# Kernel optimization log

Measured on AMD Instinct MI355X. Metric: run time of the kernel, lower is better.

## Reference

```python
import jax, jax.numpy as jnp
import numpy as np

N_HEAD = 12
D_MODEL = 768


def setup_inputs() -> dict:
    key = jax.random.key(0)
    ks = jax.random.split(key, 5)
    B, S, D = 8, 1024, D_MODEL
    return {
        "x": jax.random.normal(ks[0], (B, S, D), dtype=jnp.float32),
        "Wqkv": jax.random.normal(ks[1], (D, 3 * D), dtype=jnp.float32) * 0.02,
        "bqkv": jax.random.normal(ks[2], (3 * D,), dtype=jnp.float32) * 0.02,
        "Wproj": jax.random.normal(ks[3], (D, D), dtype=jnp.float32) * 0.02,
        "bproj": jax.random.normal(ks[4], (D,), dtype=jnp.float32) * 0.02,
    }


def _attention(x, Wqkv, bqkv, Wproj, bproj):
    B, S, D = x.shape
    hd = D // N_HEAD
    qkv = x @ Wqkv + bqkv                      # [B,S,3D]
    q, k, v = jnp.split(qkv, 3, axis=-1)
    # split heads -> [B,H,S,hd]
    def sh(t):
        return t.reshape(B, S, N_HEAD, hd).transpose(0, 2, 1, 3)
    q, k, v = sh(q), sh(k), sh(v)
    scores = jnp.einsum("bhqd,bhkd->bhqk", q, k) / jnp.sqrt(jnp.float32(hd))
    causal = jnp.tril(jnp.ones((S, S), dtype=bool))  # [S,S]
    mask_value = jnp.finfo(scores.dtype).min
    scores = jnp.where(causal[None, None], scores, mask_value)
    attn = jax.nn.softmax(scores, axis=-1)
    # dropout p=0.1 treated as identity (eval mode)
    out = jnp.einsum("bhqk,bhkd->bhqd", attn, v)
    out = out.transpose(0, 2, 1, 3).reshape(B, S, D)  # merge heads
    return out @ Wproj + bproj


def reference(x, Wqkv, bqkv, Wproj, bproj):
    return _attention(x, Wqkv, bqkv, Wproj, bproj)
```

## Files before the change

kernel.cpp:

```cpp
#include <hip/hip_runtime.h>
#include <cstddef>

typedef float f32x4 __attribute__((ext_vector_type(4)));
typedef short s16x4 __attribute__((ext_vector_type(4)));
typedef short s16x8 __attribute__((ext_vector_type(8)));
typedef __bf16 bf16x8 __attribute__((ext_vector_type(8)));

#define NB 8
#define NS 1024
#define ND 768
#define NH 12
#define HD 64

__device__ __forceinline__ unsigned short f2bf(float f) {
  unsigned u = __builtin_bit_cast(unsigned, f);
  u += 0x7fffu + ((u >> 16) & 1u);
  return (unsigned short)(u >> 16);
}

__device__ __forceinline__ f32x4 mfma16(bf16x8 a, bf16x8 b, f32x4 c) {
  return __builtin_amdgcn_mfma_f32_16x16x32_bf16(a, b, c, 0, 0, 0);
}

__device__ __forceinline__ bf16x8 ld8(const unsigned short* p) {
  return *reinterpret_cast<const bf16x8*>(p);
}

__device__ __forceinline__ void gload16(unsigned short* lds_dst, const unsigned short* gsrc) {
  __builtin_amdgcn_global_load_lds(
      (const __attribute__((address_space(1))) unsigned int*)gsrc,
      (__attribute__((address_space(3))) unsigned int*)lds_dst, 16, 0, 0);
}

#define VMW(N) asm volatile("s_waitcnt vmcnt(" #N ")" ::: "memory")


__global__ __launch_bounds__(256) void cvt_f32_bf16(const float* __restrict__ in,
                                                    unsigned short* __restrict__ out) {
  int i = (blockIdx.x * 256 + threadIdx.x) * 4;
  float4 v = *reinterpret_cast<const float4*>(in + i);
  ushort4 o;
  o.x = f2bf(v.x); o.y = f2bf(v.y); o.z = f2bf(v.z); o.w = f2bf(v.w);
  *reinterpret_cast<ushort4*>(out + i) = o;
}

__global__ __launch_bounds__(256) void transpose_cvt(const float* __restrict__ in,
                                                     unsigned short* __restrict__ out,
                                                     int R, int C) {
  __shared__ float tile[32][33];
  int c0 = blockIdx.x * 32, r0 = blockIdx.y * 32;
  int tx = threadIdx.x & 31, ty = threadIdx.x >> 5;
#pragma unroll
  for (int i = 0; i < 32; i += 8)
    tile[ty + i][tx] = in[(size_t)(r0 + ty + i) * C + c0 + tx];
  __syncthreads();
#pragma unroll
  for (int i = 0; i < 32; i += 8)
    out[(size_t)(c0 + ty + i) * R + r0 + tx] = f2bf(tile[tx][ty + i]);
}


#define SLOT 8192

__device__ __forceinline__ void gemm_mainloop4(const unsigned short* __restrict__ A,
                                               const unsigned short* __restrict__ Bt,
                                               int K, int m0, int n0,
                                               unsigned short* smem,
                                               f32x4 (&acc)[4][4]) {
  int tid = threadIdx.x, lane = tid & 63, wid = tid >> 6;
  int wr = wid >> 1, wc = wid & 1;
  int ll = lane & 15, lh = lane >> 4;
  int swsrc = ((lane & 3) ^ ((lane >> 3) & 3)) * 8;

  const unsigned short* asrc = A + (size_t)(m0 + wid * 32 + (lane >> 2)) * K + swsrc;
  const unsigned short* bsrc = Bt + (size_t)(n0 + wid * 32 + (lane >> 2)) * K + swsrc;
  const int sw = (lh ^ ((ll >> 1) & 3)) * 8;
  const int nt = K / 32;

  auto stage = [&](int slot, int t) {
    unsigned short* ad = smem + slot * SLOT + wid * 1024;
    unsigned short* bd = smem + slot * SLOT + 4096 + wid * 1024;
    const unsigned short* as = asrc + t * 32;
    const unsigned short* bs = bsrc + t * 32;
    gload16(ad, as);
    gload16(ad + 512, as + (size_t)16 * K);
    gload16(bd, bs);
    gload16(bd + 512, bs + (size_t)16 * K);
  };

  stage(0, 0);
  stage(1, 1);
  stage(2, 2);
  VMW(8);
  __builtin_amdgcn_s_barrier();
  asm volatile("" ::: "memory");

  for (int t = 0; t < nt; ++t) {
    if (t + 3 < nt) stage((t + 3) & 3, t + 3);

    const unsigned short* Ab = smem + (t & 3) * SLOT;
    const unsigned short* Bb = Ab + 4096;

    __builtin_amdgcn_s_setprio(1);
    bf16x8 af[4], bg[4];
#pragma unroll
    for (int m = 0; m < 4; m++) af[m] = ld8(Ab + (wr * 64 + m * 16 + ll) * 32 + sw);
#pragma unroll
    for (int n = 0; n < 4; n++) bg[n] = ld8(Bb + (wc * 64 + n * 16 + ll) * 32 + sw);
#pragma unroll
    for (int m = 0; m < 4; m++)
#pragma unroll
      for (int n = 0; n < 4; n++) acc[m][n] = mfma16(af[m], bg[n], acc[m][n]);
    __builtin_amdgcn_s_setprio(0);

    if (t + 3 < nt) {
      VMW(8);
      __builtin_amdgcn_s_barrier();
      asm volatile("" ::: "memory");
    } else if (t + 2 < nt) {
      VMW(4);
      __builtin_amdgcn_s_barrier();
      asm volatile("" ::: "memory");
    } else if (t + 1 < nt) {
      VMW(0);
      __builtin_amdgcn_s_barrier();
      asm volatile("" ::: "memory");
    }
  }
}

__device__ __forceinline__ void gemm_mainloop3(const unsigned short* __restrict__ A,
                                               const unsigned short* __restrict__ Bt,
                                               int K, int m0, int n0,
                                               unsigned short* smem,
                                               f32x4 (&acc)[4][4]) {
  int tid = threadIdx.x, lane = tid & 63, wid = tid >> 6;
  int wr = wid >> 1, wc = wid & 1;
  int ll = lane & 15, lh = lane >> 4;
  int swsrc = ((lane & 3) ^ ((lane >> 3) & 3)) * 8;

  const unsigned short* asrc = A + (size_t)(m0 + wid * 32 + (lane >> 2)) * K + swsrc;
  const unsigned short* bsrc = Bt + (size_t)(n0 + wid * 32 + (lane >> 2)) * K + swsrc;
  const int sw = (lh ^ ((ll >> 1) & 3)) * 8;
  const int nt = K / 32;

  auto stage = [&](int slot, int t) {
    unsigned short* ad = smem + slot * SLOT + wid * 1024;
    unsigned short* bd = smem + slot * SLOT + 4096 + wid * 1024;
    const unsigned short* as = asrc + t * 32;
    const unsigned short* bs = bsrc + t * 32;
    gload16(ad, as);
    gload16(ad + 512, as + (size_t)16 * K);
    gload16(bd, bs);
    gload16(bd + 512, bs + (size_t)16 * K);
  };

  stage(0, 0);
  stage(1, 1);
  VMW(4);
  __builtin_amdgcn_s_barrier();
  asm volatile("" ::: "memory");

  int slot = 0;
  for (int t = 0; t < nt; ++t) {
    if (t + 2 < nt) {
      int s2 = slot + 2; if (s2 >= 3) s2 -= 3;
      stage(s2, t + 2);
    }
    const unsigned short* Ab = smem + slot * SLOT;
    const unsigned short* Bb = Ab + 4096;

    __builtin_amdgcn_s_setprio(1);
    bf16x8 af[4], bg[4];
#pragma unroll
    for (int m = 0; m < 4; m++) af[m] = ld8(Ab + (wr * 64 + m * 16 + ll) * 32 + sw);
#pragma unroll
    for (int n = 0; n < 4; n++) bg[n] = ld8(Bb + (wc * 64 + n * 16 + ll) * 32 + sw);
#pragma unroll
    for (int m = 0; m < 4; m++)
#pragma unroll
      for (int n = 0; n < 4; n++) acc[m][n] = mfma16(af[m], bg[n], acc[m][n]);
    __builtin_amdgcn_s_setprio(0);

    if (t + 2 < nt) {
      VMW(4);
      __builtin_amdgcn_s_barrier();
      asm volatile("" ::: "memory");
    } else if (t + 2 == nt) {
      VMW(0);
      __builtin_amdgcn_s_barrier();
      asm volatile("" ::: "memory");
    }
    slot++; if (slot == 3) slot = 0;
  }
}


#define QSCALE 0.18033688f

__global__ __launch_bounds__(256, 2) void qkv_gemm(const unsigned short* __restrict__ xbf,
                                                   const unsigned short* __restrict__ WT,
                                                   const float* __restrict__ bias,
                                                   unsigned short* __restrict__ qw,
                                                   unsigned short* __restrict__ kw,
                                                   unsigned short* __restrict__ vt) {
  __shared__ __align__(16) unsigned short smem[4 * SLOT];
  int bid = blockIdx.x;
  int k8 = bid & 7, j = bid >> 3;
  int m0 = (k8 * 8 + (j & 7)) * 128;
  int n0 = (j >> 3) * 128;
  f32x4 acc[4][4];
#pragma unroll
  for (int m = 0; m < 4; m++)
#pragma unroll
    for (int n = 0; n < 4; n++) acc[m][n] = (f32x4){0.f, 0.f, 0.f, 0.f};

  gemm_mainloop4(xbf, WT, ND, m0, n0, smem, acc);

  int tid = threadIdx.x, lane = tid & 63, wid = tid >> 6;
  int wr = wid >> 1, wc = wid & 1;
  int ll = lane & 15, lh = lane >> 4;
  int which = n0 / ND;

  if (which == 2) {
#pragma unroll
    for (int nf = 0; nf < 4; nf++) {
      int col = n0 + wc * 64 + nf * 16 + ll;
      float bv = bias[col];
      int w2 = col - 2 * ND;
      int h = w2 >> 6, d = w2 & 63;
#pragma unroll
      for (int mf = 0; mf < 4; mf++) {
        int m = m0 + wr * 64 + mf * 16 + lh * 4;
        int b = m >> 10, s = m & 1023;
        s16x4 pk;
        pk[0] = (short)f2bf(acc[mf][nf][0] + bv);
        pk[1] = (short)f2bf(acc[mf][nf][1] + bv);
        pk[2] = (short)f2bf(acc[mf][nf][2] + bv);
        pk[3] = (short)f2bf(acc[mf][nf][3] + bv);
        size_t idx = (((size_t)b * NH + h) * HD + d) * NS + s;
        *(s16x4*)&vt[idx] = pk;
      }
    }
  } else {
#pragma unroll
    for (int nf = 0; nf < 4; nf++) {
      int col = n0 + wc * 64 + nf * 16 + ll;
      float bv = bias[col];
      int w2 = col - which * ND;
      int h = w2 >> 6, d = w2 & 63;
#pragma unroll
      for (int mf = 0; mf < 4; mf++) {
#pragma unroll
        for (int r = 0; r < 4; r++) {
          int m = m0 + wr * 64 + mf * 16 + lh * 4 + r;
          int b = m >> 10, s = m & 1023;
          float v = acc[mf][nf][r] + bv;
          size_t idx = (((size_t)b * NH + h) * NS + s) * HD + d;
          if (which == 0)
            qw[idx] = f2bf(v * QSCALE);
          else
            kw[idx] = f2bf(v);
        }
      }
    }
  }
}


__global__ __launch_bounds__(256, 3) void proj_gemm(const unsigned short* __restrict__ abf,
                                                    const unsigned short* __restrict__ WT,
                                                    const float* __restrict__ bias,
                                                    float* __restrict__ out) {
  __shared__ __align__(16) unsigned short smem[3 * SLOT];
  int bid = blockIdx.x;
  int k8 = bid & 7, j = bid >> 3;
  int m0 = (k8 * 8 + (j & 7)) * 128;
  int n0 = (j >> 3) * 128;
  f32x4 acc[4][4];
#pragma unroll
  for (int m = 0; m < 4; m++)
#pragma unroll
    for (int n = 0; n < 4; n++) acc[m][n] = (f32x4){0.f, 0.f, 0.f, 0.f};

  gemm_mainloop3(abf, WT, ND, m0, n0, smem, acc);

  int tid = threadIdx.x, lane = tid & 63, wid = tid >> 6;
  int wr = wid >> 1, wc = wid & 1;
  int ll = lane & 15, lh = lane >> 4;
#pragma unroll
  for (int nf = 0; nf < 4; nf++) {
    int col = n0 + wc * 64 + nf * 16 + ll;
    float bv = bias[col];
#pragma unroll
    for (int mf = 0; mf < 4; mf++) {
#pragma unroll
      for (int r = 0; r < 4; r++) {
        int m = m0 + wr * 64 + mf * 16 + lh * 4 + r;
        out[(size_t)m * ND + col] = acc[mf][nf][r] + bv;
      }
    }
  }
}


#define LP 88
#define KVSLOT 8192

__global__ __launch_bounds__(512) void attn_kernel(const unsigned short* __restrict__ qw,
                                                   const unsigned short* __restrict__ kw,
                                                   const unsigned short* __restrict__ vt,
                                                   unsigned short* __restrict__ attn_out) {
  int bid = blockIdx.x;
  int xcd = bid & 7, j = bid >> 3;
  int grp = xcd * 12 + (j % 12);
  int qt = 3 - (j / 12);
  int b = grp / NH, h = grp % NH;
  __shared__ __align__(16) unsigned short KV[3 * KVSLOT];
  __shared__ __align__(16) unsigned short Ps[8][16 * LP];

  int tid = threadIdx.x, lane = tid & 63, wid = tid >> 6;
  int ll = lane & 15, lh = lane >> 4, r7x = ll & 7;
  int q0 = qt * 256, q0w = q0 + wid * 32;
  const size_t bhk = ((size_t)b * NH + h) * NS * HD;
  const size_t bhv = ((size_t)b * NH + h) * HD * NS;

  bf16x8 qf[2][2];
#pragma unroll
  for (int g = 0; g < 2; g++) {
    qf[g][0] = ld8(&qw[bhk + (size_t)(q0w + g * 16 + ll) * HD + lh * 8]);
    qf[g][1] = ld8(&qw[bhk + (size_t)(q0w + g * 16 + ll) * HD + 32 + lh * 8]);
  }

  f32x4 o[2][4];
#pragma unroll
  for (int g = 0; g < 2; g++)
#pragma unroll
    for (int n = 0; n < 4; n++) o[g][n] = (f32x4){0.f, 0.f, 0.f, 0.f};
  float m_r[2] = {-1e30f, -1e30f}, l_r[2] = {0.f, 0.f};

  int srow = tid >> 3;
  int scol = ((tid & 7) ^ ((tid >> 3) & 7)) * 8;
  const unsigned short* ksrc = kw + bhk + (size_t)srow * HD + scol;
  const unsigned short* vsrc = vt + bhv + (size_t)srow * NS + scol;

  unsigned short* pw = &Ps[wid][ll * LP];
  const int qmaxw = q0w + 31;
  const int nt = 4 * (qt + 1);

  auto stage = [&](int slot, int t) {
    unsigned short* kd = KV + slot * KVSLOT + wid * 512;
    unsigned short* vd = KV + slot * KVSLOT + 4096 + wid * 512;
    gload16(kd, ksrc + (size_t)t * 64 * HD);
    gload16(vd, vsrc + t * 64);
  };

  stage(0, 0);
  stage(1, 1);
  VMW(2);
  __builtin_amdgcn_s_barrier();
  asm volatile("" ::: "memory");

  int slot = 0;
  for (int t = 0; t < nt; ++t) {
    if (t + 2 < nt) {
      int s2 = slot + 2; if (s2 >= 3) s2 -= 3;
      stage(s2, t + 2);
    }
    int j0 = t * 64;

    if (j0 <= qmaxw) {
      const unsigned short* Kb = KV + slot * KVSLOT;
      const unsigned short* Vb = Kb + 4096;

#pragma unroll
      for (int g = 0; g < 2; g++) {
        f32x4 sa[4];
#pragma unroll
        for (int n = 0; n < 4; n++) {
          bf16x8 kf0 = ld8(Kb + (n * 16 + ll) * 64 + (lh ^ r7x) * 8);
          bf16x8 kf1 = ld8(Kb + (n * 16 + ll) * 64 + ((4 + lh) ^ r7x) * 8);
          sa[n] = mfma16(kf0, qf[g][0], (f32x4){0.f, 0.f, 0.f, 0.f});
          sa[n] = mfma16(kf1, qf[g][1], sa[n]);
        }

        int qbase = q0w + g * 16;
        if (j0 + 63 > qbase) {
          int qme = qbase + ll;
#pragma unroll
          for (int n = 0; n < 4; n++)
#pragma unroll
            for (int r = 0; r < 4; r++)
              if (j0 + n * 16 + lh * 4 + r > qme) sa[n][r] = -1e30f;
        }

        float t0 = fmaxf(fmaxf(sa[0][0], sa[0][1]), fmaxf(sa[0][2], sa[0][3]));
        float t1 = fmaxf(fmaxf(sa[1][0], sa[1][1]), fmaxf(sa[1][2], sa[1][3]));
        float t2 = fmaxf(fmaxf(sa[2][0], sa[2][1]), fmaxf(sa[2][2], sa[2][3]));
        float t3 = fmaxf(fmaxf(sa[3][0], sa[3][1]), fmaxf(sa[3][2], sa[3][3]));
        float tmax = fmaxf(fmaxf(t0, t1), fmaxf(t2, t3));
        tmax = fmaxf(tmax, __shfl_xor(tmax, 16));
        tmax = fmaxf(tmax, __shfl_xor(tmax, 32));

        if (!__all(tmax - m_r[g] <= 11.5f)) {
          float mnew = fmaxf(m_r[g], tmax);
          float alpha = exp2f(m_r[g] - mnew);
          m_r[g] = mnew;
          l_r[g] *= alpha;
          float ab0 = __shfl(alpha, lh * 4 + 0);
          float ab1 = __shfl(alpha, lh * 4 + 1);
          float ab2 = __shfl(alpha, lh * 4 + 2);
          float ab3 = __shfl(alpha, lh * 4 + 3);
#pragma unroll
          for (int n2 = 0; n2 < 4; n2++) {
            o[g][n2][0] *= ab0; o[g][n2][1] *= ab1;
            o[g][n2][2] *= ab2; o[g][n2][3] *= ab3;
          }
        }

        float p[4][4];
        float ssum = 0.f;
#pragma unroll
        for (int n = 0; n < 4; n++)
#pragma unroll
          for (int r = 0; r < 4; r++) {
            p[n][r] = exp2f(sa[n][r] - m_r[g]);
            ssum += p[n][r];
          }
        ssum += __shfl_xor(ssum, 16);
        ssum += __shfl_xor(ssum, 32);
        l_r[g] += ssum;

#pragma unroll
        for (int n = 0; n < 4; n++) {
          s16x4 pk;
          pk[0] = (short)f2bf(p[n][0]);
          pk[1] = (short)f2bf(p[n][1]);
          pk[2] = (short)f2bf(p[n][2]);
          pk[3] = (short)f2bf(p[n][3]);
          *(s16x4*)&pw[n * 16 + lh * 4] = pk;
        }

#pragma unroll
        for (int c = 0; c < 2; c++) {
          bf16x8 pf = ld8(&pw[c * 32 + lh * 8]);
#pragma unroll
          for (int n2 = 0; n2 < 4; n2++) {
            bf16x8 vf = ld8(Vb + (n2 * 16 + ll) * 64 + ((c * 4 + lh) ^ r7x) * 8);
            o[g][n2] = mfma16(pf, vf, o[g][n2]);
          }
        }
      }
    }

    if (t + 2 < nt) {
      VMW(2);
      __builtin_amdgcn_s_barrier();
      asm volatile("" ::: "memory");
    } else if (t + 2 == nt) {
      VMW(0);
      __builtin_amdgcn_s_barrier();
      asm volatile("" ::: "memory");
    }
    slot++; if (slot == 3) slot = 0;
  }

#pragma unroll
  for (int g = 0; g < 2; g++) {
    float lrec = 1.0f / l_r[g];
    float lb0 = __shfl(lrec, lh * 4 + 0);
    float lb1 = __shfl(lrec, lh * 4 + 1);
    float lb2 = __shfl(lrec, lh * 4 + 2);
    float lb3 = __shfl(lrec, lh * 4 + 3);
#pragma unroll
    for (int n2 = 0; n2 < 4; n2++) {
      int d = n2 * 16 + ll;
      int qb = q0w + g * 16 + lh * 4;
      attn_out[((size_t)b * NS + qb + 0) * ND + h * HD + d] = f2bf(o[g][n2][0] * lb0);
      attn_out[((size_t)b * NS + qb + 1) * ND + h * HD + d] = f2bf(o[g][n2][1] * lb1);
      attn_out[((size_t)b * NS + qb + 2) * ND + h * HD + d] = f2bf(o[g][n2][2] * lb2);
      attn_out[((size_t)b * NS + qb + 3) * ND + h * HD + d] = f2bf(o[g][n2][3] * lb3);
    }
  }
}


extern "C" void kernel_launch(void* const* d_in, const int* in_sizes, int n_in,
                              void* d_out, int out_size, void* d_ws, size_t ws_size,
                              hipStream_t stream) {
  const float* x = (const float*)d_in[0];
  const float* Wqkv = (const float*)d_in[1];
  const float* bqkv = (const float*)d_in[2];
  const float* Wproj = (const float*)d_in[3];
  const float* bproj = (const float*)d_in[4];
  float* out = (float*)d_out;

  char* ws = (char*)d_ws;
  const size_t SZ_X = (size_t)NB * NS * ND * 2;
  const size_t SZ_WQKV = (size_t)ND * 3 * ND * 2;
  const size_t SZ_WPROJ = (size_t)ND * ND * 2;
  const size_t SZ_HEAD = (size_t)NB * NH * NS * HD;

  unsigned short* xbf = (unsigned short*)(ws);
  unsigned short* wqkvT = (unsigned short*)(ws + SZ_X);
  unsigned short* wprojT = (unsigned short*)(ws + SZ_X + SZ_WQKV);
  unsigned short* qw = (unsigned short*)(ws + SZ_X + SZ_WQKV + SZ_WPROJ);
  unsigned short* kw = qw + SZ_HEAD;
  unsigned short* vt = kw + SZ_HEAD;
  unsigned short* attn = vt + SZ_HEAD;

  (void)in_sizes; (void)n_in; (void)out_size; (void)ws_size;

  cvt_f32_bf16<<<(NB * NS * ND) / 1024, 256, 0, stream>>>(x, xbf);
  transpose_cvt<<<dim3(3 * ND / 32, ND / 32), 256, 0, stream>>>(Wqkv, wqkvT, ND, 3 * ND);
  transpose_cvt<<<dim3(ND / 32, ND / 32), 256, 0, stream>>>(Wproj, wprojT, ND, ND);

  qkv_gemm<<<1152, 256, 0, stream>>>(xbf, wqkvT, bqkv, qw, kw, vt);

  attn_kernel<<<384, 512, 0, stream>>>(qw, kw, vt, attn);

  proj_gemm<<<384, 256, 0, stream>>>(attn, wprojT, bproj, out);
}
```

Baseline: 122.8 us.

## Pair early and late causal query tiles per block to balance attention work

Each attention block now handles two 128-row query tiles, one from the late half and its mirror from the early half, in place of one contiguous 256-row tile. Each wave owns 16 rows from each tile, and the causal skip is decided per group. Every block therefore does a similar amount of causal work, which removes the tail where blocks on the last query tiles run much longer than those on the first. In exchange, blocks with short early tiles stream as many K/V tiles as their late tile needs, and waves sit idle on the early group once past its diagonal.

```diff
diff --git a/kernel.cpp b/kernel.cpp
--- a/kernel.cpp
+++ b/kernel.cpp
@@ -314,22 +314,24 @@
   int bid = blockIdx.x;
   int xcd = bid & 7, j = bid >> 3;
   int grp = xcd * 12 + (j % 12);
-  int qt = 3 - (j / 12);
+  int p = j / 12;
+  int qtA = 4 + p, qtB = 3 - p;
   int b = grp / NH, h = grp % NH;
   __shared__ __align__(16) unsigned short KV[3 * KVSLOT];
   __shared__ __align__(16) unsigned short Ps[8][16 * LP];
 
   int tid = threadIdx.x, lane = tid & 63, wid = tid >> 6;
   int ll = lane & 15, lh = lane >> 4, r7x = ll & 7;
-  int q0 = qt * 256, q0w = q0 + wid * 32;
   const size_t bhk = ((size_t)b * NH + h) * NS * HD;
   const size_t bhv = ((size_t)b * NH + h) * HD * NS;
 
+  int q0w[2] = {qtA * 128 + wid * 16, qtB * 128 + wid * 16};
+
   bf16x8 qf[2][2];
 #pragma unroll
   for (int g = 0; g < 2; g++) {
-    qf[g][0] = ld8(&qw[bhk + (size_t)(q0w + g * 16 + ll) * HD + lh * 8]);
-    qf[g][1] = ld8(&qw[bhk + (size_t)(q0w + g * 16 + ll) * HD + 32 + lh * 8]);
+    qf[g][0] = ld8(&qw[bhk + (size_t)(q0w[g] + ll) * HD + lh * 8]);
+    qf[g][1] = ld8(&qw[bhk + (size_t)(q0w[g] + ll) * HD + 32 + lh * 8]);
   }
 
   f32x4 o[2][4];
@@ -345,8 +347,7 @@
   const unsigned short* vsrc = vt + bhv + (size_t)srow * NS + scol;
 
   unsigned short* pw = &Ps[wid][ll * LP];
-  const int qmaxw = q0w + 31;
-  const int nt = 4 * (qt + 1);
+  const int nt = 2 * (qtA + 1);
 
   auto stage = [&](int slot, int t) {
     unsigned short* kd = KV + slot * KVSLOT + wid * 512;
@@ -368,13 +369,12 @@
       stage(s2, t + 2);
     }
     int j0 = t * 64;
-
-    if (j0 <= qmaxw) {
-      const unsigned short* Kb = KV + slot * KVSLOT;
-      const unsigned short* Vb = Kb + 4096;
-
-#pragma unroll
-      for (int g = 0; g < 2; g++) {
+    const unsigned short* Kb = KV + slot * KVSLOT;
+    const unsigned short* Vb = Kb + 4096;
+
+#pragma unroll
+    for (int g = 0; g < 2; g++) {
+      if (j0 <= q0w[g] + 15) {
         f32x4 sa[4];
 #pragma unroll
         for (int n = 0; n < 4; n++) {
@@ -384,9 +384,8 @@
           sa[n] = mfma16(kf1, qf[g][1], sa[n]);
         }
 
-        int qbase = q0w + g * 16;
-        if (j0 + 63 > qbase) {
-          int qme = qbase + ll;
+        if (j0 + 63 > q0w[g]) {
+          int qme = q0w[g] + ll;
 #pragma unroll
           for (int n = 0; n < 4; n++)
 #pragma unroll
@@ -418,14 +417,14 @@
           }
         }
 
-        float p[4][4];
+        float pv[4][4];
         float ssum = 0.f;
 #pragma unroll
         for (int n = 0; n < 4; n++)
 #pragma unroll
           for (int r = 0; r < 4; r++) {
-            p[n][r] = exp2f(sa[n][r] - m_r[g]);
-            ssum += p[n][r];
+            pv[n][r] = exp2f(sa[n][r] - m_r[g]);
+            ssum += pv[n][r];
           }
         ssum += __shfl_xor(ssum, 16);
         ssum += __shfl_xor(ssum, 32);
@@ -434,10 +433,10 @@
 #pragma unroll
         for (int n = 0; n < 4; n++) {
           s16x4 pk;
-          pk[0] = (short)f2bf(p[n][0]);
-          pk[1] = (short)f2bf(p[n][1]);
-          pk[2] = (short)f2bf(p[n][2]);
-          pk[3] = (short)f2bf(p[n][3]);
+          pk[0] = (short)f2bf(pv[n][0]);
+          pk[1] = (short)f2bf(pv[n][1]);
+          pk[2] = (short)f2bf(pv[n][2]);
+          pk[3] = (short)f2bf(pv[n][3]);
           *(s16x4*)&pw[n * 16 + lh * 4] = pk;
         }
 
@@ -475,7 +474,7 @@
 #pragma unroll
     for (int n2 = 0; n2 < 4; n2++) {
       int d = n2 * 16 + ll;
-      int qb = q0w + g * 16 + lh * 4;
+      int qb = q0w[g] + lh * 4;
       attn_out[((size_t)b * NS + qb + 0) * ND + h * HD + d] = f2bf(o[g][n2][0] * lb0);
       attn_out[((size_t)b * NS + qb + 1) * ND + h * HD + d] = f2bf(o[g][n2][1] * lb1);
       attn_out[((size_t)b * NS + qb + 2) * ND + h * HD + d] = f2bf(o[g][n2][2] * lb2);
```

Measured after the change: 122.3 us. About the same (-0.4%).
